# Kernel optimization log

Measured on AMD Instinct MI355X. Metric: run time of the kernel, lower is better.

Reference implementation:

```python
import jax, jax.numpy as jnp
import numpy as np

D = 256
H = 8
DK = D // H
FF = 4 * D
EPS = 1e-5


def layer_norm(x, g, b):
    mu = jnp.mean(x, axis=-1, keepdims=True)
    var = jnp.mean(jnp.square(x - mu), axis=-1, keepdims=True)
    return (x - mu) * jax.lax.rsqrt(var + EPS) * g + b


def setup_inputs() -> dict:
    key = jax.random.key(0)
    ks = jax.random.split(key, 12)
    s = 0.02
    return {
        "x": jax.random.normal(ks[0], (4, 2048, D), jnp.float32),
        "Wq": jax.random.normal(ks[1], (D, D), jnp.float32) * s,
        "Wk": jax.random.normal(ks[2], (D, D), jnp.float32) * s,
        "Wv": jax.random.normal(ks[3], (D, D), jnp.float32) * s,
        "Wo": jax.random.normal(ks[4], (D, D), jnp.float32) * s,
        "W1": jax.random.normal(ks[5], (D, FF), jnp.float32) * s,
        "W2": jax.random.normal(ks[6], (D, FF), jnp.float32) * s,
        "Wout": jax.random.normal(ks[7], (FF, D), jnp.float32) * s,
        "g1": jnp.ones((D,), jnp.float32),
        "b1": jnp.zeros((D,), jnp.float32),
        "g2": jnp.ones((D,), jnp.float32),
        "b2": jnp.zeros((D,), jnp.float32),
    }


def reference(x, Wq, Wk, Wv, Wo, W1, W2, Wout, g1, b1, g2, b2):
    B, S, _ = x.shape
    # --- multi-head attention (manual matmul + softmax + matmul) ---
    q = (x @ Wq).reshape(B, S, H, DK).transpose(0, 2, 1, 3)  # [B,H,S,DK]
    k = (x @ Wk).reshape(B, S, H, DK).transpose(0, 2, 1, 3)
    v = (x @ Wv).reshape(B, S, H, DK).transpose(0, 2, 1, 3)
    scores = jnp.einsum("bhqd,bhkd->bhqk", q, k) * (DK ** -0.5)  # [B,H,S,S]
    probs = jax.nn.softmax(scores, axis=-1)
    o = jnp.einsum("bhqk,bhkd->bhqd", probs, v)
    attn = o.transpose(0, 2, 1, 3).reshape(B, S, D) @ Wo
    # --- GLU feedforward with dual LayerNorms ---
    x1 = layer_norm(x + attn, g1, b1)
    xw = jax.nn.silu(x1 @ W1)
    xv = x1 @ W2
    out = (xw * xv) @ Wout
    return layer_norm(x1 + out, g2, b2)
```

## Files before the change

### kernel.cpp

```cpp
#include <hip/hip_runtime.h>

#define D 256
#define H 8
#define DK 32
#define FF 1024
#define SEQ 2048
#define BATCH 4
#define MROWS (BATCH * SEQ)
#define LN_EPS 1e-5f
#define QSCALE (0.1767766952966369f * 1.4426950408889634f)

typedef unsigned short u16;
typedef unsigned int u32;
typedef __attribute__((ext_vector_type(8))) short bf16x8;
typedef __attribute__((ext_vector_type(4))) float f32x4;

#define MFMA16(a, b, c) __builtin_amdgcn_mfma_f32_16x16x32_bf16(a, b, c, 0, 0, 0)

__device__ __forceinline__ u16 f2bf(float f) {
    union { float f; u32 u; } x; x.f = f;
    u32 r = x.u + 0x7fffu + ((x.u >> 16) & 1u);
    return (u16)(r >> 16);
}
__device__ __forceinline__ u32 pack2(float a, float b) {
    return (u32)f2bf(a) | ((u32)f2bf(b) << 16);
}
__device__ __forceinline__ u32 pktrunc(float a, float b) {
    u32 ua = __builtin_bit_cast(u32, a), ub = __builtin_bit_cast(u32, b);
    return __builtin_amdgcn_perm(ub, ua, 0x07060302u);
}

__global__ void stage_w(const float* __restrict__ Wq, const float* __restrict__ Wk,
                        const float* __restrict__ Wv, const float* __restrict__ Wo,
                        const float* __restrict__ W1, const float* __restrict__ W2,
                        const float* __restrict__ Wout, u16* __restrict__ dst) {
    __shared__ float T[64][65];
    int bid = blockIdx.x, tid = threadIdx.x;
    const float* src;
    size_t dbase;
    int K, N, tile;
    float sc = 1.f;
    if (bid < 64) {
        int which = bid >> 4;
        tile = bid & 15;
        src = which == 0 ? Wq : which == 1 ? Wk : which == 2 ? Wv : Wo;
        if (which == 0) sc = QSCALE;
        dbase = (size_t)which << 16;
        K = 256; N = 256;
    } else if (bid < 192) {
        int which = (bid - 64) >> 6;
        tile = (bid - 64) & 63;
        src = which ? W2 : W1;
        dbase = 262144 + (size_t)which * 262144;
        K = 256; N = 1024;
    } else {
        tile = bid - 192;
        src = Wout;
        dbase = 786432;
        K = 1024; N = 256;
    }
    int ntn = N >> 6;
    int k0 = (tile / ntn) << 6, n0 = (tile % ntn) << 6;
#pragma unroll
    for (int p = 0; p < 4; p++) {
        int r = p * 16 + (tid >> 4), c = (tid & 15) * 4;
        float4 v = *(const float4*)(src + (size_t)(k0 + r) * N + n0 + c);
        T[c + 0][r] = v.x * sc;
        T[c + 1][r] = v.y * sc;
        T[c + 2][r] = v.z * sc;
        T[c + 3][r] = v.w * sc;
    }
    __syncthreads();
#pragma unroll
    for (int p = 0; p < 4; p++) {
        int n = p * 16 + (tid >> 4), k = (tid & 15) * 4;
        uint2 o;
        o.x = pack2(T[n][k], T[n][k + 1]);
        o.y = pack2(T[n][k + 2], T[n][k + 3]);
        *(uint2*)(dst + dbase + (size_t)(n0 + n) * K + k0 + k) = o;
    }
}

__global__ void gemm_qkv(const float* __restrict__ X, const u16* __restrict__ Bt,
                         u16* __restrict__ Qo, u16* __restrict__ Ko,
                         u16* __restrict__ Vo) {
    int gid = (blockIdx.x * 256 + threadIdx.x) >> 6;
    int lane = threadIdx.x & 63;
    int mt = gid / 12, ng = gid - mt * 12;
    int m0 = mt << 5, n0 = ng << 6;
    int m = lane & 15, quad = lane >> 4;
    const float* xp0 = X + (size_t)(m0 + m) * D + quad * 8;
    const float* xp1 = xp0 + (size_t)16 * D;
    const u16* bp = Bt + (size_t)(n0 + m) * D + quad * 8;
    f32x4 acc[2][4] = {{{0,0,0,0},{0,0,0,0},{0,0,0,0},{0,0,0,0}},
                       {{0,0,0,0},{0,0,0,0},{0,0,0,0},{0,0,0,0}}};
    for (int k0 = 0; k0 < D; k0 += 32) {
        float4 f0 = *(const float4*)(xp0 + k0);
        float4 f1 = *(const float4*)(xp0 + k0 + 4);
        float4 f2 = *(const float4*)(xp1 + k0);
        float4 f3 = *(const float4*)(xp1 + k0 + 4);
        uint4 u0, u1;
        u0.x = pktrunc(f0.x, f0.y); u0.y = pktrunc(f0.z, f0.w);
        u0.z = pktrunc(f1.x, f1.y); u0.w = pktrunc(f1.z, f1.w);
        u1.x = pktrunc(f2.x, f2.y); u1.y = pktrunc(f2.z, f2.w);
        u1.z = pktrunc(f3.x, f3.y); u1.w = pktrunc(f3.z, f3.w);
        bf16x8 a0 = __builtin_bit_cast(bf16x8, u0);
        bf16x8 a1 = __builtin_bit_cast(bf16x8, u1);
#pragma unroll
        for (int t = 0; t < 4; t++) {
            bf16x8 bv = *(const bf16x8*)(bp + (size_t)t * 16 * D + k0);
            acc[0][t] = MFMA16(a0, bv, acc[0][t]);
            acc[1][t] = MFMA16(a1, bv, acc[1][t]);
        }
    }
    int seg = n0 >> 8;
    int nc0 = n0 & 255;
    if (seg < 2) {
        u16* out = seg ? Ko : Qo;
#pragma unroll
        for (int u = 0; u < 2; u++) {
            int row = m0 + u * 16 + (quad << 2);
#pragma unroll
            for (int t = 0; t < 4; t++) {
                int col = nc0 + t * 16 + m;
#pragma unroll
                for (int r = 0; r < 4; r++)
                    out[(size_t)(row + r) * D + col] = f2bf(acc[u][t][r]);
            }
        }
    } else {
#pragma unroll
        for (int u = 0; u < 2; u++) {
            int row = m0 + u * 16 + (quad << 2);
            int b = row >> 11, sl = row & 2047;
#pragma unroll
            for (int t = 0; t < 4; t++) {
                int col = nc0 + t * 16 + m;
                int hh = col >> 5, dk = col & 31;
                size_t base = ((size_t)(b * 8 + hh) * 32 + dk) * SEQ + sl;
                uint2 pk;
                pk.x = pack2(acc[u][t][0], acc[u][t][1]);
                pk.y = pack2(acc[u][t][2], acc[u][t][3]);
                *(uint2*)(Vo + base) = pk;
            }
        }
    }
}

__global__ __launch_bounds__(256, 8)
void attn_mfma(const u16* __restrict__ Q, const u16* __restrict__ Km,
               const u16* __restrict__ Vt, u16* __restrict__ O) {
    __shared__ __align__(16) u16 Kt[2][64][36];
    __shared__ __align__(16) u16 Vl[2][32][68];
    int tid = threadIdx.x;
    int lane = tid & 63;
    int m = lane & 15, quad = lane >> 4;
    int w = tid >> 6;
    int bid = blockIdx.x;
    int qb = bid & 63;
    int bh = bid >> 6;
    int b = bh >> 3, h = bh & 7;
    int q0 = qb * 32 + (w & 1) * 16;
    int hb = w >> 1;
    size_t rowbase = (size_t)b * SEQ;

    bf16x8 qa = *(const bf16x8*)(Q + (rowbase + q0 + m) * D + h * DK + quad * 8);

    const u16* kg = Km + rowbase * D + h * DK;
    const u16* vg = Vt + (size_t)bh * DK * SEQ;

    int krow = tid >> 2, kseg = tid & 3;
    int skv = (krow & 32) | (((krow >> 2) & 3) << 3) | (((krow >> 4) & 1) << 2) | (krow & 3);
    int vrow = tid >> 3, vseg = tid & 7;

    uint4 kreg = *(const uint4*)(kg + (size_t)skv * D + kseg * 8);
    uint4 vreg = *(const uint4*)(vg + (size_t)vrow * SEQ + vseg * 8);
    *(uint4*)(&Kt[0][krow][kseg * 8]) = kreg;
    *(uint4*)(&Vl[0][vrow][vseg * 8]) = vreg;

    f32x4 o0 = {0,0,0,0}, o1 = {0,0,0,0};
    float ls = 0.f;

    for (int i = 0; i < SEQ / 64; i++) {
        int buf = i & 1;
        if (i + 1 < SEQ / 64) {
            int kvn = (i + 1) * 64;
            kreg = *(const uint4*)(kg + (size_t)(kvn + skv) * D + kseg * 8);
            vreg = *(const uint4*)(vg + (size_t)vrow * SEQ + kvn + vseg * 8);
        }
        __syncthreads();
        f32x4 z = {0,0,0,0};
        f32x4 s0, s1;
        {
            bf16x8 kb0 = *(const bf16x8*)(&Kt[buf][(2 * hb) * 16 + m][quad * 8]);
            bf16x8 kb1 = *(const bf16x8*)(&Kt[buf][(2 * hb + 1) * 16 + m][quad * 8]);
            s0 = MFMA16(kb0, qa, z);
            s1 = MFMA16(kb1, qa, z);
        }
        {
            float pa0 = exp2f(s0[0]), pa1 = exp2f(s0[1]);
            float pa2 = exp2f(s0[2]), pa3 = exp2f(s0[3]);
            float pb0 = exp2f(s1[0]), pb1 = exp2f(s1[1]);
            float pb2 = exp2f(s1[2]), pb3 = exp2f(s1[3]);
            ls += ((pa0 + pa1) + (pa2 + pa3)) + ((pb0 + pb1) + (pb2 + pb3));
            uint4 pw;
            pw.x = pktrunc(pa0, pa1);
            pw.y = pktrunc(pa2, pa3);
            pw.z = pktrunc(pb0, pb1);
            pw.w = pktrunc(pb2, pb3);
            bf16x8 pfrag = __builtin_bit_cast(bf16x8, pw);
            bf16x8 vb0 = *(const bf16x8*)(&Vl[buf][m][hb * 32 + quad * 8]);
            bf16x8 vb1 = *(const bf16x8*)(&Vl[buf][16 + m][hb * 32 + quad * 8]);
            o0 = MFMA16(pfrag, vb0, o0);
            o1 = MFMA16(pfrag, vb1, o1);
        }
        if (i + 1 < SEQ / 64) {
            *(uint4*)(&Kt[buf ^ 1][krow][kseg * 8]) = kreg;
            *(uint4*)(&Vl[buf ^ 1][vrow][vseg * 8]) = vreg;
        }
    }
    ls += __shfl_xor(ls, 16);
    ls += __shfl_xor(ls, 32);
    __syncthreads();
    float* comb = (float*)&Kt[0][0][0];
    if (w >= 2) {
        float* c = comb + ((size_t)(w - 2) * 64 + lane) * 9;
#pragma unroll
        for (int r = 0; r < 4; r++) { c[r] = o0[r]; c[4 + r] = o1[r]; }
        c[8] = ls;
    }
    __syncthreads();
    if (w < 2) {
        const float* c = comb + ((size_t)w * 64 + lane) * 9;
#pragma unroll
        for (int r = 0; r < 4; r++) { o0[r] += c[r]; o1[r] += c[4 + r]; }
        ls += c[8];
        u16* ob = O + (rowbase + q0 + quad * 4) * D + h * DK;
#pragma unroll
        for (int r = 0; r < 4; r++) {
            float lr = __shfl(ls, quad * 4 + r);
            float inv = 1.f / lr;
            ob[(size_t)r * D + m] = f2bf(o0[r] * inv);
            ob[(size_t)r * D + 16 + m] = f2bf(o1[r] * inv);
        }
    }
}

__global__ __launch_bounds__(256, 2)
void wo_res_ln(const u16* __restrict__ A, const u16* __restrict__ Bt,
               const float* __restrict__ res, const float* __restrict__ g,
               const float* __restrict__ bb, float* __restrict__ outf) {
    __shared__ float Sy[4][16], Sq[4][16], Mu[16], Rs[16];
    int tid = threadIdx.x;
    int w = tid >> 6, lane = tid & 63;
    int m = lane & 15, quad = lane >> 4;
    int m0 = blockIdx.x << 4, n0 = w << 6;
    const u16* ap = A + (size_t)(m0 + m) * D + quad * 8;
    const u16* bp = Bt + (size_t)(n0 + m) * D + quad * 8;
    f32x4 acc[4] = {{0,0,0,0},{0,0,0,0},{0,0,0,0},{0,0,0,0}};
#pragma unroll
    for (int k0 = 0; k0 < D; k0 += 32) {
        bf16x8 a0 = *(const bf16x8*)(ap + k0);
#pragma unroll
        for (int t = 0; t < 4; t++)
            acc[t] = MFMA16(a0, *(const bf16x8*)(bp + (size_t)t * 16 * D + k0), acc[t]);
    }
#pragma unroll
    for (int r = 0; r < 4; r++) {
        int row = (quad << 2) + r;
        float sy = 0.f, sq = 0.f;
#pragma unroll
        for (int t = 0; t < 4; t++) {
            float y = acc[t][r] + res[(size_t)(m0 + row) * D + n0 + t * 16 + m];
            acc[t][r] = y;
            sy += y;
            sq += y * y;
        }
        sy += __shfl_xor(sy, 1); sq += __shfl_xor(sq, 1);
        sy += __shfl_xor(sy, 2); sq += __shfl_xor(sq, 2);
        sy += __shfl_xor(sy, 4); sq += __shfl_xor(sq, 4);
        sy += __shfl_xor(sy, 8); sq += __shfl_xor(sq, 8);
        if (m == 0) { Sy[w][row] = sy; Sq[w][row] = sq; }
    }
    __syncthreads();
    if (tid < 16) {
        float s = Sy[0][tid] + Sy[1][tid] + Sy[2][tid] + Sy[3][tid];
        float q = Sq[0][tid] + Sq[1][tid] + Sq[2][tid] + Sq[3][tid];
        float mu = s * (1.f / 256.f);
        float var = q * (1.f / 256.f) - mu * mu;
        Mu[tid] = mu;
        Rs[tid] = rsqrtf(var + LN_EPS);
    }
    __syncthreads();
#pragma unroll
    for (int r = 0; r < 4; r++) {
        int row = (quad << 2) + r;
        float mu = Mu[row], rs = Rs[row];
#pragma unroll
        for (int t = 0; t < 4; t++) {
            int col = n0 + t * 16 + m;
            outf[(size_t)(m0 + row) * D + col] = (acc[t][r] - mu) * rs * g[col] + bb[col];
        }
    }
}

__global__ __launch_bounds__(512, 2)
void ff_fused(const float* __restrict__ x1f, const u16* __restrict__ W1t,
              const u16* __restrict__ W2t, const u16* __restrict__ Woutt,
              const float* __restrict__ g, const float* __restrict__ bb,
              float* __restrict__ outf) {
    __shared__ __align__(16) u16 X1l[32][268];
    __shared__ __align__(16) u16 Gl[32][1044];
    __shared__ float Sy[8][32], Sq[8][32], Mu[32], Rs[32];
    int tid = threadIdx.x;
    int w = tid >> 6, lane = tid & 63;
    int m = lane & 15, quad = lane >> 4;
    int m0 = blockIdx.x << 5;

#pragma unroll
    for (int p = 0; p < 4; p++) {
        int idx = p * 512 + tid;
        int row = idx >> 6, c = (idx & 63) * 4;
        float4 v = *(const float4*)(x1f + (size_t)(m0 + row) * D + c);
        uint2 o;
        o.x = pack2(v.x, v.y);
        o.y = pack2(v.z, v.w);
        *(uint2*)(&X1l[row][c]) = o;
    }
    __syncthreads();

#pragma unroll
    for (int i = 0; i < 2; i++) {
        int n0 = (w * 2 + i) << 6;
        const u16* b1 = W1t + (size_t)(n0 + m) * D + quad * 8;
        const u16* b2 = W2t + (size_t)(n0 + m) * D + quad * 8;
        f32x4 a1[2][4] = {{{0,0,0,0},{0,0,0,0},{0,0,0,0},{0,0,0,0}},
                          {{0,0,0,0},{0,0,0,0},{0,0,0,0},{0,0,0,0}}};
        f32x4 a2[2][4] = {{{0,0,0,0},{0,0,0,0},{0,0,0,0},{0,0,0,0}},
                          {{0,0,0,0},{0,0,0,0},{0,0,0,0},{0,0,0,0}}};
#pragma unroll
        for (int k0 = 0; k0 < D; k0 += 32) {
            bf16x8 av0 = *(const bf16x8*)(&X1l[m][k0 + quad * 8]);
            bf16x8 av1 = *(const bf16x8*)(&X1l[16 + m][k0 + quad * 8]);
#pragma unroll
            for (int t = 0; t < 4; t++) {
                bf16x8 w1 = *(const bf16x8*)(b1 + (size_t)t * 16 * D + k0);
                bf16x8 w2 = *(const bf16x8*)(b2 + (size_t)t * 16 * D + k0);
                a1[0][t] = MFMA16(av0, w1, a1[0][t]);
                a1[1][t] = MFMA16(av1, w1, a1[1][t]);
                a2[0][t] = MFMA16(av0, w2, a2[0][t]);
                a2[1][t] = MFMA16(av1, w2, a2[1][t]);
            }
        }
#pragma unroll
        for (int u = 0; u < 2; u++) {
            int row = u * 16 + (quad << 2);
#pragma unroll
            for (int t = 0; t < 4; t++) {
                int col = n0 + t * 16 + m;
#pragma unroll
                for (int r = 0; r < 4; r++) {
                    float wv = a1[u][t][r];
                    float s = wv / (1.f + __expf(-wv));
                    Gl[row + r][col] = f2bf(s * a2[u][t][r]);
                }
            }
        }
    }
    __syncthreads();

    int n0p = w << 5;
    const u16* bp = Woutt + (size_t)(n0p + m) * FF + quad * 8;
    f32x4 acc[2][2] = {{{0,0,0,0},{0,0,0,0}},{{0,0,0,0},{0,0,0,0}}};
    for (int k0 = 0; k0 < FF; k0 += 32) {
        bf16x8 a0 = *(const bf16x8*)(&Gl[m][k0 + quad * 8]);
        bf16x8 a1v = *(const bf16x8*)(&Gl[16 + m][k0 + quad * 8]);
#pragma unroll
        for (int t = 0; t < 2; t++) {
            bf16x8 bv = *(const bf16x8*)(bp + (size_t)t * 16 * FF + k0);
            acc[0][t] = MFMA16(a0, bv, acc[0][t]);
            acc[1][t] = MFMA16(a1v, bv, acc[1][t]);
        }
    }
#pragma unroll
    for (int u = 0; u < 2; u++) {
#pragma unroll
        for (int r = 0; r < 4; r++) {
            int row = u * 16 + (quad << 2) + r;
            float sy = 0.f, sq = 0.f;
#pragma unroll
            for (int t = 0; t < 2; t++) {
                float y = acc[u][t][r] +
                          x1f[(size_t)(m0 + row) * D + n0p + t * 16 + m];
                acc[u][t][r] = y;
                sy += y;
                sq += y * y;
            }
            sy += __shfl_xor(sy, 1); sq += __shfl_xor(sq, 1);
            sy += __shfl_xor(sy, 2); sq += __shfl_xor(sq, 2);
            sy += __shfl_xor(sy, 4); sq += __shfl_xor(sq, 4);
            sy += __shfl_xor(sy, 8); sq += __shfl_xor(sq, 8);
            if (m == 0) { Sy[w][row] = sy; Sq[w][row] = sq; }
        }
    }
    __syncthreads();
    if (tid < 32) {
        float s = 0.f, q = 0.f;
#pragma unroll
        for (int ww = 0; ww < 8; ww++) { s += Sy[ww][tid]; q += Sq[ww][tid]; }
        float mu = s * (1.f / 256.f);
        float var = q * (1.f / 256.f) - mu * mu;
        Mu[tid] = mu;
        Rs[tid] = rsqrtf(var + LN_EPS);
    }
    __syncthreads();
#pragma unroll
    for (int u = 0; u < 2; u++) {
#pragma unroll
        for (int r = 0; r < 4; r++) {
            int row = u * 16 + (quad << 2) + r;
            float mu = Mu[row], rs = Rs[row];
#pragma unroll
            for (int t = 0; t < 2; t++) {
                int col = n0p + t * 16 + m;
                outf[(size_t)(m0 + row) * D + col] =
                    (acc[u][t][r] - mu) * rs * g[col] + bb[col];
            }
        }
    }
}

#define WS_WQKVT  ((size_t)0)
#define WS_WOT    ((size_t)196608)
#define WS_W1T    ((size_t)262144)
#define WS_W2T    ((size_t)524288)
#define WS_WOUTT  ((size_t)786432)
#define WS_Q      ((size_t)1048576)
#define WS_K      ((size_t)3145728)
#define WS_VT     ((size_t)5242880)
#define WS_O      ((size_t)7340032)
#define WS_X1F    ((size_t)9437184)

extern "C" void kernel_launch(void* const* d_in, const int* in_sizes, int n_in,
                              void* d_out, int out_size, void* d_ws, size_t ws_size,
                              hipStream_t stream) {
    const float* x    = (const float*)d_in[0];
    const float* Wq   = (const float*)d_in[1];
    const float* Wk   = (const float*)d_in[2];
    const float* Wv   = (const float*)d_in[3];
    const float* Wo   = (const float*)d_in[4];
    const float* W1   = (const float*)d_in[5];
    const float* W2   = (const float*)d_in[6];
    const float* Wout = (const float*)d_in[7];
    const float* g1   = (const float*)d_in[8];
    const float* b1   = (const float*)d_in[9];
    const float* g2   = (const float*)d_in[10];
    const float* b2   = (const float*)d_in[11];

    u16* ws = (u16*)d_ws;
    float* x1f = (float*)(ws + WS_X1F);

    stage_w<<<256, 256, 0, stream>>>(Wq, Wk, Wv, Wo, W1, W2, Wout, ws + WS_WQKVT);

    gemm_qkv<<<768, 256, 0, stream>>>(x, ws + WS_WQKVT,
                                      ws + WS_Q, ws + WS_K, ws + WS_VT);

    attn_mfma<<<2048, 256, 0, stream>>>(ws + WS_Q, ws + WS_K, ws + WS_VT, ws + WS_O);

    wo_res_ln<<<512, 256, 0, stream>>>(ws + WS_O, ws + WS_WOT, x, g1, b1, x1f);

    ff_fused<<<256, 512, 0, stream>>>(x1f, ws + WS_W1T, ws + WS_W2T, ws + WS_WOUTT,
                                      g2, b2, (float*)d_out);
}
```

Before: 216.4 us.

## Shrink fused FFN row tile to 16 rows with 256-thread blocks

Switches the fused GLU feedforward kernel from 32-row tiles in 512-thread blocks to 16-row tiles in 256-thread blocks, so it launches 512 blocks instead of 256. Each wave now covers more output columns with a single A row-fragment. The goal is to fill more of the GPU's compute units and cut LDS and register use per block. The cost is that each weight fragment read from global or L2 now feeds only one MFMA instead of two, which doubles total weight traffic.

```diff
diff --git a/kernel.cpp b/kernel.cpp
--- a/kernel.cpp
+++ b/kernel.cpp
@@ -304,22 +304,22 @@
     }
 }
 
-__global__ __launch_bounds__(512, 2)
+__global__ __launch_bounds__(256, 3)
 void ff_fused(const float* __restrict__ x1f, const u16* __restrict__ W1t,
               const u16* __restrict__ W2t, const u16* __restrict__ Woutt,
               const float* __restrict__ g, const float* __restrict__ bb,
               float* __restrict__ outf) {
-    __shared__ __align__(16) u16 X1l[32][268];
-    __shared__ __align__(16) u16 Gl[32][1044];
-    __shared__ float Sy[8][32], Sq[8][32], Mu[32], Rs[32];
+    __shared__ __align__(16) u16 X1l[16][268];
+    __shared__ __align__(16) u16 Gl[16][1044];
+    __shared__ float Sy[4][16], Sq[4][16], Mu[16], Rs[16];
     int tid = threadIdx.x;
     int w = tid >> 6, lane = tid & 63;
     int m = lane & 15, quad = lane >> 4;
-    int m0 = blockIdx.x << 5;
+    int m0 = blockIdx.x << 4;
 
 #pragma unroll
     for (int p = 0; p < 4; p++) {
-        int idx = p * 512 + tid;
+        int idx = p * 256 + tid;
         int row = idx >> 6, c = (idx & 63) * 4;
         float4 v = *(const float4*)(x1f + (size_t)(m0 + row) * D + c);
         uint2 o;
@@ -330,84 +330,64 @@
     __syncthreads();
 
 #pragma unroll
-    for (int i = 0; i < 2; i++) {
-        int n0 = (w * 2 + i) << 6;
+    for (int i = 0; i < 4; i++) {
+        int n0 = (w * 4 + i) << 6;
         const u16* b1 = W1t + (size_t)(n0 + m) * D + quad * 8;
         const u16* b2 = W2t + (size_t)(n0 + m) * D + quad * 8;
-        f32x4 a1[2][4] = {{{0,0,0,0},{0,0,0,0},{0,0,0,0},{0,0,0,0}},
-                          {{0,0,0,0},{0,0,0,0},{0,0,0,0},{0,0,0,0}}};
-        f32x4 a2[2][4] = {{{0,0,0,0},{0,0,0,0},{0,0,0,0},{0,0,0,0}},
-                          {{0,0,0,0},{0,0,0,0},{0,0,0,0},{0,0,0,0}}};
+        f32x4 a1[4] = {{0,0,0,0},{0,0,0,0},{0,0,0,0},{0,0,0,0}};
+        f32x4 a2[4] = {{0,0,0,0},{0,0,0,0},{0,0,0,0},{0,0,0,0}};
 #pragma unroll
         for (int k0 = 0; k0 < D; k0 += 32) {
-            bf16x8 av0 = *(const bf16x8*)(&X1l[m][k0 + quad * 8]);
-            bf16x8 av1 = *(const bf16x8*)(&X1l[16 + m][k0 + quad * 8]);
+            bf16x8 av = *(const bf16x8*)(&X1l[m][k0 + quad * 8]);
 #pragma unroll
             for (int t = 0; t < 4; t++) {
-                bf16x8 w1 = *(const bf16x8*)(b1 + (size_t)t * 16 * D + k0);
-                bf16x8 w2 = *(const bf16x8*)(b2 + (size_t)t * 16 * D + k0);
-                a1[0][t] = MFMA16(av0, w1, a1[0][t]);
-                a1[1][t] = MFMA16(av1, w1, a1[1][t]);
-                a2[0][t] = MFMA16(av0, w2, a2[0][t]);
-                a2[1][t] = MFMA16(av1, w2, a2[1][t]);
+                a1[t] = MFMA16(av, *(const bf16x8*)(b1 + (size_t)t * 16 * D + k0), a1[t]);
+                a2[t] = MFMA16(av, *(const bf16x8*)(b2 + (size_t)t * 16 * D + k0), a2[t]);
             }
         }
 #pragma unroll
-        for (int u = 0; u < 2; u++) {
-            int row = u * 16 + (quad << 2);
-#pragma unroll
-            for (int t = 0; t < 4; t++) {
-                int col = n0 + t * 16 + m;
-#pragma unroll
-                for (int r = 0; r < 4; r++) {
-                    float wv = a1[u][t][r];
-                    float s = wv / (1.f + __expf(-wv));
-                    Gl[row + r][col] = f2bf(s * a2[u][t][r]);
-                }
+        for (int t = 0; t < 4; t++) {
+            int col = n0 + t * 16 + m;
+#pragma unroll
+            for (int r = 0; r < 4; r++) {
+                float wv = a1[t][r];
+                float s = wv / (1.f + __expf(-wv));
+                Gl[(quad << 2) + r][col] = f2bf(s * a2[t][r]);
             }
         }
     }
     __syncthreads();
 
-    int n0p = w << 5;
+    int n0p = w << 6;
     const u16* bp = Woutt + (size_t)(n0p + m) * FF + quad * 8;
-    f32x4 acc[2][2] = {{{0,0,0,0},{0,0,0,0}},{{0,0,0,0},{0,0,0,0}}};
+    f32x4 acc[4] = {{0,0,0,0},{0,0,0,0},{0,0,0,0},{0,0,0,0}};
     for (int k0 = 0; k0 < FF; k0 += 32) {
         bf16x8 a0 = *(const bf16x8*)(&Gl[m][k0 + quad * 8]);
-        bf16x8 a1v = *(const bf16x8*)(&Gl[16 + m][k0 + quad * 8]);
-#pragma unroll
-        for (int t = 0; t < 2; t++) {
-            bf16x8 bv = *(const bf16x8*)(bp + (size_t)t * 16 * FF + k0);
-            acc[0][t] = MFMA16(a0, bv, acc[0][t]);
-            acc[1][t] = MFMA16(a1v, bv, acc[1][t]);
-        }
-    }
-#pragma unroll
-    for (int u = 0; u < 2; u++) {
-#pragma unroll
-        for (int r = 0; r < 4; r++) {
-            int row = u * 16 + (quad << 2) + r;
-            float sy = 0.f, sq = 0.f;
-#pragma unroll
-            for (int t = 0; t < 2; t++) {
-                float y = acc[u][t][r] +
-                          x1f[(size_t)(m0 + row) * D + n0p + t * 16 + m];
-                acc[u][t][r] = y;
-                sy += y;
-                sq += y * y;
-            }
-            sy += __shfl_xor(sy, 1); sq += __shfl_xor(sq, 1);
-            sy += __shfl_xor(sy, 2); sq += __shfl_xor(sq, 2);
-            sy += __shfl_xor(sy, 4); sq += __shfl_xor(sq, 4);
-            sy += __shfl_xor(sy, 8); sq += __shfl_xor(sq, 8);
-            if (m == 0) { Sy[w][row] = sy; Sq[w][row] = sq; }
-        }
-    }
-    __syncthreads();
-    if (tid < 32) {
-        float s = 0.f, q = 0.f;
-#pragma unroll
-        for (int ww = 0; ww < 8; ww++) { s += Sy[ww][tid]; q += Sq[ww][tid]; }
+#pragma unroll
+        for (int t = 0; t < 4; t++)
+            acc[t] = MFMA16(a0, *(const bf16x8*)(bp + (size_t)t * 16 * FF + k0), acc[t]);
+    }
+#pragma unroll
+    for (int r = 0; r < 4; r++) {
+        int row = (quad << 2) + r;
+        float sy = 0.f, sq = 0.f;
+#pragma unroll
+        for (int t = 0; t < 4; t++) {
+            float y = acc[t][r] + x1f[(size_t)(m0 + row) * D + n0p + t * 16 + m];
+            acc[t][r] = y;
+            sy += y;
+            sq += y * y;
+        }
+        sy += __shfl_xor(sy, 1); sq += __shfl_xor(sq, 1);
+        sy += __shfl_xor(sy, 2); sq += __shfl_xor(sq, 2);
+        sy += __shfl_xor(sy, 4); sq += __shfl_xor(sq, 4);
+        sy += __shfl_xor(sy, 8); sq += __shfl_xor(sq, 8);
+        if (m == 0) { Sy[w][row] = sy; Sq[w][row] = sq; }
+    }
+    __syncthreads();
+    if (tid < 16) {
+        float s = Sy[0][tid] + Sy[1][tid] + Sy[2][tid] + Sy[3][tid];
+        float q = Sq[0][tid] + Sq[1][tid] + Sq[2][tid] + Sq[3][tid];
         float mu = s * (1.f / 256.f);
         float var = q * (1.f / 256.f) - mu * mu;
         Mu[tid] = mu;
@@ -415,17 +395,14 @@
     }
     __syncthreads();
 #pragma unroll
-    for (int u = 0; u < 2; u++) {
-#pragma unroll
-        for (int r = 0; r < 4; r++) {
-            int row = u * 16 + (quad << 2) + r;
-            float mu = Mu[row], rs = Rs[row];
-#pragma unroll
-            for (int t = 0; t < 2; t++) {
-                int col = n0p + t * 16 + m;
-                outf[(size_t)(m0 + row) * D + col] =
-                    (acc[u][t][r] - mu) * rs * g[col] + bb[col];
-            }
+    for (int r = 0; r < 4; r++) {
+        int row = (quad << 2) + r;
+        float mu = Mu[row], rs = Rs[row];
+#pragma unroll
+        for (int t = 0; t < 4; t++) {
+            int col = n0p + t * 16 + m;
+            outf[(size_t)(m0 + row) * D + col] =
+                (acc[t][r] - mu) * rs * g[col] + bb[col];
         }
     }
 }
@@ -469,6 +446,6 @@
 
     wo_res_ln<<<512, 256, 0, stream>>>(ws + WS_O, ws + WS_WOT, x, g1, b1, x1f);
 
-    ff_fused<<<256, 512, 0, stream>>>(x1f, ws + WS_W1T, ws + WS_W2T, ws + WS_WOUTT,
+    ff_fused<<<512, 256, 0, stream>>>(x1f, ws + WS_W1T, ws + WS_W2T, ws + WS_WOUTT,
                                       g2, b2, (float*)d_out);
 }
```

New measurement: 253.8 us. 1.17x slower.
